# Performance work log

Hardware: AMD Instinct MI355X
Metric: run time of the kernel (lower is better)

The kernel has to match this reference:

```python
import jax, jax.numpy as jnp
import numpy as np

N = 20000   # nodes
E = 320000  # edges
F = 64      # input node features
H = 256     # hidden_layer_size
C = 10      # nbr_classes
G = 64      # graphs in the batch


def _lin(key, fan_in, fan_out):
    k1, k2 = jax.random.split(key)
    bound = 1.0 / np.sqrt(fan_in)
    W = jax.random.uniform(k1, (fan_in, fan_out), jnp.float32, -bound, bound)
    b = jax.random.uniform(k2, (fan_out,), jnp.float32, -bound, bound)
    return W, b


def setup_inputs() -> dict:
    key = jax.random.key(0)
    ks = jax.random.split(key, 10)
    x = jax.random.normal(ks[0], (N, F), jnp.float32)
    edge_index = jax.random.randint(ks[1], (2, E), 0, N)
    batch = jnp.sort(jax.random.randint(ks[2], (N,), 0, G))
    W1, b1 = _lin(ks[3], F, H)
    W2, b2 = _lin(ks[4], H, H)
    W3, b3 = _lin(ks[5], H, H)
    W4, b4 = _lin(ks[6], H, H)
    W5, b5 = _lin(ks[7], H, H)
    Wout, bout = _lin(ks[8], H, C)
    return {"x": x, "edge_index": edge_index, "batch": batch,
            "W1": W1, "b1": b1, "W2": W2, "b2": b2, "W3": W3, "b3": b3,
            "W4": W4, "b4": b4, "W5": W5, "b5": b5, "Wout": Wout, "bout": bout}


def reference(x, edge_index, batch, W1, b1, W2, b2, W3, b3, W4, b4, W5, b5, Wout, bout):
    # GCNConv (Kipf & Welling): add self-loops, D^{-1/2}(A+I)D^{-1/2} (X W) + b.
    # Dropout(p=0.5) is identity in eval mode (reference is deterministic).
    loop = jnp.arange(N)
    row = jnp.concatenate([edge_index[0], loop])  # source nodes, [E+N]
    col = jnp.concatenate([edge_index[1], loop])  # target nodes, [E+N]
    deg = jax.ops.segment_sum(jnp.ones(E + N, x.dtype), col, num_segments=N)
    dinv = jax.lax.rsqrt(deg)  # deg >= 1 thanks to self-loops
    norm = (dinv[row] * dinv[col])[:, None]  # [E+N, 1]

    def gcn_conv(h, W, b):
        m = (h @ W)[row] * norm                      # gather + normalize, [E+N, H]
        return jax.ops.segment_sum(m, col, num_segments=N) + b

    h = x
    for W, b in ((W1, b1), (W2, b2), (W3, b3), (W4, b4), (W5, b5)):
        h = jax.nn.relu(gcn_conv(h, W, b))

    # global_mean_pool over graph ids
    counts = jax.ops.segment_sum(jnp.ones(N, h.dtype), batch, num_segments=G)
    pooled = jax.ops.segment_sum(h, batch, num_segments=G) / jnp.maximum(counts, 1.0)[:, None]
    return pooled @ Wout + bout  # [G, C]
```

## Files before the change

kernel.cpp:

```cpp
#include <hip/hip_runtime.h>

#define NN 20000
#define NE 320000
#define FIN 64
#define HD 256
#define NC 10
#define NG 64
#define NB ((NN + 255) / 256)
#define EBMAX (NE + 15 * NN + 16)

typedef unsigned short u16;
typedef unsigned int u32;
typedef __attribute__((ext_vector_type(8))) short short8;
typedef __attribute__((ext_vector_type(4))) float f32x4;

__device__ __forceinline__ float bf2f(u16 u) {
    union { u32 i; float f; } v; v.i = ((u32)u) << 16; return v.f;
}
__device__ __forceinline__ u16 f2bf(float f) {
    union { float f; u32 i; } v; v.f = f;
    u32 r = v.i + 0x7fffu + ((v.i >> 16) & 1u);
    return (u16)(r >> 16);
}

__global__ void k_deg(const int* __restrict__ col, int* __restrict__ degi,
                      const int* __restrict__ batch, int* __restrict__ gstart) {
    int i = blockIdx.x * 256 + threadIdx.x;
    if (i < NE) atomicAdd(&degi[col[i]], 1);
    if (i < NN) {
        int b = batch[i];
        int prev = (i == 0) ? -1 : batch[i - 1];
        if (b != prev) gstart[b] = i;
    }
}

__global__ void k_pad(u32* __restrict__ ebuf32) {
    int i = blockIdx.x * 256 + threadIdx.x;
    if (i < EBMAX / 2) ebuf32[i] = 0x4E204E20u;
}

__global__ __launch_bounds__(256) void k_scan1(const int* __restrict__ degi,
                                               int* __restrict__ rowptr,
                                               int* __restrict__ bsum) {
    int t = threadIdx.x;
    int i = blockIdx.x * 256 + t;
    int v = (i < NN) ? ((degi[i] + 15) & ~15) : 0;
    int lane = t & 63, wid = t >> 6;
    int x = v;
#pragma unroll
    for (int off = 1; off < 64; off <<= 1) {
        int y = __shfl_up(x, off);
        if (lane >= off) x += y;
    }
    __shared__ int ws[4];
    if (lane == 63) ws[wid] = x;
    __syncthreads();
    int woff = 0;
    for (int w = 0; w < wid; ++w) woff += ws[w];
    if (i < NN) rowptr[i] = woff + x - v;
    if (t == 255) bsum[blockIdx.x] = woff + x;
}

__global__ void k_scan3(const int* __restrict__ degi, const int* __restrict__ bsum,
                        int* __restrict__ rowptr, int* __restrict__ cursor,
                        float* __restrict__ dinv,
                        const float* __restrict__ x, u16* __restrict__ u0) {
    __shared__ int pref[NB];
    if (threadIdx.x < NB) pref[threadIdx.x] = bsum[threadIdx.x];
    __syncthreads();
    if (threadIdx.x == 0) {
        int run = 0;
        for (int k = 0; k < NB; ++k) { int t = pref[k]; pref[k] = run; run += t; }
    }
    __syncthreads();
    int i = blockIdx.x * 256 + threadIdx.x;
    if (i < NN) {
        int dg = degi[i];
        int rp = rowptr[i] + pref[i >> 8];
        rowptr[i] = rp;
        cursor[i] = rp;
        dinv[i] = rsqrtf((float)(1 + dg));
        if (i == NN - 1) rowptr[NN] = rp + ((dg + 15) & ~15);
    }
    if (i < NN * FIN / 4) {
        int node = i >> 4;
        float d = rsqrtf((float)(1 + degi[node]));
        float4 v = *(const float4*)&x[(size_t)i * 4];
        u32 lo = (u32)f2bf(v.x * d) | ((u32)f2bf(v.y * d) << 16);
        u32 hi = (u32)f2bf(v.z * d) | ((u32)f2bf(v.w * d) << 16);
        *(uint2*)&u0[(size_t)i * 4] = make_uint2(lo, hi);
    }
    if (blockIdx.x == 0 && threadIdx.x < FIN) u0[(size_t)NN * FIN + threadIdx.x] = 0;
}

__global__ void k_fill(const int* __restrict__ row, const int* __restrict__ col,
                       int* __restrict__ cursor, u16* __restrict__ ebuf) {
    int e = blockIdx.x * 256 + threadIdx.x;
    if (e < NE) {
        int c = col[e];
        int pos = atomicAdd(&cursor[c], 1);
        ebuf[pos] = (u16)row[e];
    }
}

__global__ __launch_bounds__(256) void k_trans(const float* __restrict__ W0, const float* __restrict__ W1,
                                               const float* __restrict__ W2, const float* __restrict__ W3,
                                               const float* __restrict__ W4,
                                               u16* __restrict__ T0, u16* __restrict__ T1,
                                               u16* __restrict__ T2, u16* __restrict__ T3,
                                               u16* __restrict__ T4) {
    int l = blockIdx.z;
    const float* W = (l == 0) ? W0 : (l == 1) ? W1 : (l == 2) ? W2 : (l == 3) ? W3 : W4;
    u16* T = (l == 0) ? T0 : (l == 1) ? T1 : (l == 2) ? T2 : (l == 3) ? T3 : T4;
    int K = (l == 0) ? FIN : HD;
    int k0 = blockIdx.x * 32;
    if (k0 >= K) return;
    int n0 = blockIdx.y * 32;
    __shared__ float tile[32][33];
    int tx = threadIdx.x & 31, ty = threadIdx.x >> 5;
#pragma unroll
    for (int r = 0; r < 32; r += 8)
        tile[ty + r][tx] = W[(size_t)(k0 + ty + r) * HD + n0 + tx];
    __syncthreads();
#pragma unroll
    for (int r = 0; r < 32; r += 8)
        T[(size_t)(n0 + ty + r) * K + k0 + tx] = f2bf(tile[tx][ty + r]);
}

__global__ __launch_bounds__(256) void k_gatherh(const u16* __restrict__ U,
                                                 const int* __restrict__ rowptr,
                                                 const u16* __restrict__ ebuf,
                                                 const float* __restrict__ dinv,
                                                 u16* __restrict__ Z) {
    int b = blockIdx.x;
    int half = b & 1;
    int tile = b >> 1;
    int n = tile * 4 + (threadIdx.x >> 6);
    if (n >= NN) return;
    int lane = threadIdx.x & 63;
    int grp = lane >> 4;
    int seg = lane & 15;
    int fbase = half * 128 + seg * 8;
    int s = rowptr[n], e = rowptr[n + 1];
    float acc[8];
    if (grp == 0) {
        uint4 v = *(const uint4*)&U[(size_t)n * HD + fbase];
        acc[0] = bf2f((u16)(v.x & 0xffff)); acc[1] = bf2f((u16)(v.x >> 16));
        acc[2] = bf2f((u16)(v.y & 0xffff)); acc[3] = bf2f((u16)(v.y >> 16));
        acc[4] = bf2f((u16)(v.z & 0xffff)); acc[5] = bf2f((u16)(v.z >> 16));
        acc[6] = bf2f((u16)(v.w & 0xffff)); acc[7] = bf2f((u16)(v.w >> 16));
    } else {
#pragma unroll
        for (int k = 0; k < 8; ++k) acc[k] = 0.f;
    }
    for (int j = s; j < e; j += 16) {
        int myid = (lane < 16) ? (int)ebuf[j + lane] : 0;
        uint4 v[4];
#pragma unroll
        for (int k = 0; k < 4; ++k) {
            int r = __shfl(myid, grp * 4 + k);
            v[k] = *(const uint4*)&U[(size_t)r * HD + fbase];
        }
#pragma unroll
        for (int k = 0; k < 4; ++k) {
            acc[0] += bf2f((u16)(v[k].x & 0xffff)); acc[1] += bf2f((u16)(v[k].x >> 16));
            acc[2] += bf2f((u16)(v[k].y & 0xffff)); acc[3] += bf2f((u16)(v[k].y >> 16));
            acc[4] += bf2f((u16)(v[k].z & 0xffff)); acc[5] += bf2f((u16)(v[k].z >> 16));
            acc[6] += bf2f((u16)(v[k].w & 0xffff)); acc[7] += bf2f((u16)(v[k].w >> 16));
        }
    }
#pragma unroll
    for (int k = 0; k < 8; ++k) {
        acc[k] += __shfl_xor(acc[k], 16);
        acc[k] += __shfl_xor(acc[k], 32);
    }
    if (grp == 0) {
        float d = dinv[n];
        uint4 o;
        o.x = (u32)f2bf(acc[0] * d) | ((u32)f2bf(acc[1] * d) << 16);
        o.y = (u32)f2bf(acc[2] * d) | ((u32)f2bf(acc[3] * d) << 16);
        o.z = (u32)f2bf(acc[4] * d) | ((u32)f2bf(acc[5] * d) << 16);
        o.w = (u32)f2bf(acc[6] * d) | ((u32)f2bf(acc[7] * d) << 16);
        *(uint4*)&Z[(size_t)n * HD + fbase] = o;
    }
}

__global__ __launch_bounds__(256) void k_gather64(const u16* __restrict__ U,
                                                  const int* __restrict__ rowptr,
                                                  const u16* __restrict__ ebuf,
                                                  const float* __restrict__ dinv,
                                                  u16* __restrict__ Z) {
    int n = blockIdx.x * 4 + (threadIdx.x >> 6);
    if (n >= NN) return;
    int lane = threadIdx.x & 63;
    int grp = lane >> 3;
    int seg = lane & 7;
    int s = rowptr[n], e = rowptr[n + 1];
    float acc[8];
    if (grp == 0) {
        uint4 v = *(const uint4*)&U[(size_t)n * FIN + seg * 8];
        acc[0] = bf2f((u16)(v.x & 0xffff)); acc[1] = bf2f((u16)(v.x >> 16));
        acc[2] = bf2f((u16)(v.y & 0xffff)); acc[3] = bf2f((u16)(v.y >> 16));
        acc[4] = bf2f((u16)(v.z & 0xffff)); acc[5] = bf2f((u16)(v.z >> 16));
        acc[6] = bf2f((u16)(v.w & 0xffff)); acc[7] = bf2f((u16)(v.w >> 16));
    } else {
#pragma unroll
        for (int k = 0; k < 8; ++k) acc[k] = 0.f;
    }
    for (int j = s; j < e; j += 16) {
        int r0 = (int)ebuf[j + grp];
        int r1 = (int)ebuf[j + 8 + grp];
        uint4 v0 = *(const uint4*)&U[(size_t)r0 * FIN + seg * 8];
        uint4 v1 = *(const uint4*)&U[(size_t)r1 * FIN + seg * 8];
        acc[0] += bf2f((u16)(v0.x & 0xffff)); acc[1] += bf2f((u16)(v0.x >> 16));
        acc[2] += bf2f((u16)(v0.y & 0xffff)); acc[3] += bf2f((u16)(v0.y >> 16));
        acc[4] += bf2f((u16)(v0.z & 0xffff)); acc[5] += bf2f((u16)(v0.z >> 16));
        acc[6] += bf2f((u16)(v0.w & 0xffff)); acc[7] += bf2f((u16)(v0.w >> 16));
        acc[0] += bf2f((u16)(v1.x & 0xffff)); acc[1] += bf2f((u16)(v1.x >> 16));
        acc[2] += bf2f((u16)(v1.y & 0xffff)); acc[3] += bf2f((u16)(v1.y >> 16));
        acc[4] += bf2f((u16)(v1.z & 0xffff)); acc[5] += bf2f((u16)(v1.z >> 16));
        acc[6] += bf2f((u16)(v1.w & 0xffff)); acc[7] += bf2f((u16)(v1.w >> 16));
    }
#pragma unroll
    for (int off = 8; off < 64; off <<= 1)
#pragma unroll
        for (int k = 0; k < 8; ++k) acc[k] += __shfl_xor(acc[k], off);
    if (grp == 0) {
        float d = dinv[n];
        uint4 o;
        o.x = (u32)f2bf(acc[0] * d) | ((u32)f2bf(acc[1] * d) << 16);
        o.y = (u32)f2bf(acc[2] * d) | ((u32)f2bf(acc[3] * d) << 16);
        o.z = (u32)f2bf(acc[4] * d) | ((u32)f2bf(acc[5] * d) << 16);
        o.w = (u32)f2bf(acc[6] * d) | ((u32)f2bf(acc[7] * d) << 16);
        *(uint4*)&Z[(size_t)n * FIN + seg * 8] = o;
    }
}

__global__ __launch_bounds__(256) void k_mm(const u16* __restrict__ A,
                                            const u16* __restrict__ Wt,
                                            const float* __restrict__ bias,
                                            const float* __restrict__ dinv,
                                            u16* __restrict__ O,
                                            int K, int scaleOut) {
    __shared__ u16 Asm[64][40];
    __shared__ u16 Bsm[256][40];
    __shared__ float bs[HD];
    const int m0 = blockIdx.x * 64;
    const int t = threadIdx.x;
    const int wave = t >> 6;
    const int lane = t & 63;
    const int quad = lane >> 4;
    const int l16 = lane & 15;
    const int n0 = wave * 64;
    bs[t] = bias[t];
    if (blockIdx.x == 0) O[(size_t)NN * HD + t] = 0;

    f32x4 acc[4][4];
#pragma unroll
    for (int i = 0; i < 4; ++i)
#pragma unroll
        for (int j = 0; j < 4; ++j) acc[i][j] = (f32x4){0.f, 0.f, 0.f, 0.f};

    for (int k0 = 0; k0 < K; k0 += 32) {
        {
            int row = t >> 2, seg = t & 3;
            int gm = m0 + row;
            float4 v = make_float4(0.f, 0.f, 0.f, 0.f);
            if (gm < NN) v = *(const float4*)&A[(size_t)gm * K + k0 + seg * 8];
            *(float4*)&Asm[row][seg * 8] = v;
        }
        {
#pragma unroll
            for (int j = 0; j < 4; ++j) {
                float4 v = *(const float4*)&Wt[(size_t)t * K + k0 + j * 8];
                *(float4*)&Bsm[t][j * 8] = v;
            }
        }
        __syncthreads();
        short8 a[4], b[4];
#pragma unroll
        for (int i = 0; i < 4; ++i) a[i] = *(const short8*)&Asm[i * 16 + l16][quad * 8];
#pragma unroll
        for (int j = 0; j < 4; ++j) b[j] = *(const short8*)&Bsm[n0 + j * 16 + l16][quad * 8];
#pragma unroll
        for (int i = 0; i < 4; ++i)
#pragma unroll
            for (int j = 0; j < 4; ++j)
                acc[i][j] = __builtin_amdgcn_mfma_f32_16x16x32_bf16(a[i], b[j], acc[i][j], 0, 0, 0);
        __syncthreads();
    }
#pragma unroll
    for (int i = 0; i < 4; ++i) {
#pragma unroll
        for (int r = 0; r < 4; ++r) {
            int m = m0 + i * 16 + quad * 4 + r;
            if (m >= NN) continue;
            float d = scaleOut ? dinv[m] : 1.0f;
#pragma unroll
            for (int j = 0; j < 4; ++j) {
                int n = n0 + j * 16 + l16;
                float val = fmaxf(acc[i][j][r] + bs[n], 0.f) * d;
                O[(size_t)m * HD + n] = f2bf(val);
            }
        }
    }
}

__global__ __launch_bounds__(256) void k_poolout(const u16* __restrict__ h,
                                                 const int* __restrict__ gstart,
                                                 const float* __restrict__ Wout,
                                                 const float* __restrict__ bout,
                                                 float* __restrict__ out) {
    int g = blockIdx.x;
    int t = threadIdx.x;
    __shared__ float pooled[HD];
    __shared__ float part[NC][16];
    __shared__ int s_se[2];
    if (t == 0) {
        int st = gstart[g];
        int en = NN;
        for (int gg = g + 1; gg < NG; ++gg) en = min(en, gstart[gg]);
        s_se[0] = st; s_se[1] = en;
    }
    __syncthreads();
    int st = s_se[0], en = s_se[1];
    float a0 = 0.f, a1 = 0.f, a2 = 0.f, a3 = 0.f;
    int n = st;
    for (; n + 4 <= en; n += 4) {
        a0 += bf2f(h[(size_t)n * HD + t]);
        a1 += bf2f(h[(size_t)(n + 1) * HD + t]);
        a2 += bf2f(h[(size_t)(n + 2) * HD + t]);
        a3 += bf2f(h[(size_t)(n + 3) * HD + t]);
    }
    for (; n < en; ++n) a0 += bf2f(h[(size_t)n * HD + t]);
    float inv = 1.0f / (float)max(en - st, 1);
    pooled[t] = (a0 + a1 + a2 + a3) * inv;
    __syncthreads();
    if (t < NC * 16) {
        int c = t >> 4, l16 = t & 15;
        float s = 0.f;
        for (int f = l16; f < HD; f += 16)
            s = fmaf(pooled[f], Wout[(size_t)f * NC + c], s);
        part[c][l16] = s;
    }
    __syncthreads();
    if (t < NC) {
        float s = 0.f;
#pragma unroll
        for (int k = 0; k < 16; ++k) s += part[t][k];
        out[(size_t)g * NC + t] = s + bout[t];
    }
}

extern "C" void kernel_launch(void* const* d_in, const int* in_sizes, int n_in,
                              void* d_out, int out_size, void* d_ws, size_t ws_size,
                              hipStream_t stream) {
    const float* x     = (const float*)d_in[0];
    const int*   ei    = (const int*)d_in[1];
    const int*   batch = (const int*)d_in[2];
    const float* Wl[5] = {(const float*)d_in[3], (const float*)d_in[5], (const float*)d_in[7],
                          (const float*)d_in[9], (const float*)d_in[11]};
    const float* bl[5] = {(const float*)d_in[4], (const float*)d_in[6], (const float*)d_in[8],
                          (const float*)d_in[10], (const float*)d_in[12]};
    const float* Wout = (const float*)d_in[13];
    const float* bout = (const float*)d_in[14];
    float* out = (float*)d_out;

    const int* row = ei;
    const int* col = ei + NE;

    char* p = (char*)d_ws;
    auto take = [&](size_t bytes) { char* q = p; p += (bytes + 255) & ~(size_t)255; return q; };
    float* dinv   = (float*)take(NN * 4);
    int*   degi   = (int*)take(NN * 4);
    int*   rowptr = (int*)take((NN + 1) * 4);
    int*   cursor = (int*)take(NN * 4);
    int*   bsum   = (int*)take(NB * 4);
    u16*   ebuf   = (u16*)take(EBMAX * 2);
    int*   gstart = (int*)take(NG * 4);
    u16*   Wt[5];
    for (int l = 0; l < 5; ++l) Wt[l] = (u16*)take((size_t)HD * HD * 2);
    u16*   B1     = (u16*)take((size_t)(NN + 1) * HD * 2);
    u16*   B2     = (u16*)take((size_t)(NN + 1) * HD * 2);

    hipMemsetAsync(degi, 0, NN * 4, stream);
    hipMemsetAsync(gstart, 0x7F, NG * 4, stream);
    k_deg<<<(NE + 255) / 256, 256, 0, stream>>>(col, degi, batch, gstart);
    k_pad<<<(EBMAX / 2 + 255) / 256, 256, 0, stream>>>((u32*)ebuf);
    k_scan1<<<NB, 256, 0, stream>>>(degi, rowptr, bsum);
    k_scan3<<<(NN * FIN / 4 + 255) / 256, 256, 0, stream>>>(degi, bsum, rowptr, cursor, dinv, x, B1);
    k_fill<<<(NE + 255) / 256, 256, 0, stream>>>(row, col, cursor, ebuf);
    dim3 tGrid(8, 8, 5);
    k_trans<<<tGrid, 256, 0, stream>>>(Wl[0], Wl[1], Wl[2], Wl[3], Wl[4],
                                       Wt[0], Wt[1], Wt[2], Wt[3], Wt[4]);

    k_gather64<<<(NN + 3) / 4, 256, 0, stream>>>(B1, rowptr, ebuf, dinv, B2);
    k_mm<<<(NN + 63) / 64, 256, 0, stream>>>(B2, Wt[0], bl[0], dinv, B1, FIN, 1);
    const int gGrid = 2 * ((NN + 3) / 4);
    for (int l = 1; l < 5; ++l) {
        k_gatherh<<<gGrid, 256, 0, stream>>>(B1, rowptr, ebuf, dinv, B2);
        k_mm<<<(NN + 63) / 64, 256, 0, stream>>>(B2, Wt[l], bl[l], dinv, B1, HD, (l < 4) ? 1 : 0);
    }

    k_poolout<<<NG, 256, 0, stream>>>(B1, gstart, Wout, bout, out);
}
```

Baseline: 347.7 us.

## Split pooling across feature tiles and replace pad kernel with memset

The fused pool+output kernel (one block per graph) becomes a pool kernel over a graph×feature-tile grid with four node-strided row partials, followed by a separate small output kernel using one wave per (graph, class). The padding kernel for the edge buffer is replaced by a byte memset to 0x4E, so padded entries point at a dummy row index 0x4E4E = 20046 (DROW) that is zeroed and allocated. This is meant to raise parallelism in the pooling tail and drop one kernel launch, at the cost of an extra launch for the output GEMV and an intermediate pooled buffer.

```diff
diff --git a/kernel.cpp b/kernel.cpp
--- a/kernel.cpp
+++ b/kernel.cpp
@@ -8,6 +8,7 @@
 #define NG 64
 #define NB ((NN + 255) / 256)
 #define EBMAX (NE + 15 * NN + 16)
+#define DROW 20046
 
 typedef unsigned short u16;
 typedef unsigned int u32;
@@ -34,11 +35,6 @@
     }
 }
 
-__global__ void k_pad(u32* __restrict__ ebuf32) {
-    int i = blockIdx.x * 256 + threadIdx.x;
-    if (i < EBMAX / 2) ebuf32[i] = 0x4E204E20u;
-}
-
 __global__ __launch_bounds__(256) void k_scan1(const int* __restrict__ degi,
                                                int* __restrict__ rowptr,
                                                int* __restrict__ bsum) {
@@ -90,7 +86,7 @@
         u32 hi = (u32)f2bf(v.z * d) | ((u32)f2bf(v.w * d) << 16);
         *(uint2*)&u0[(size_t)i * 4] = make_uint2(lo, hi);
     }
-    if (blockIdx.x == 0 && threadIdx.x < FIN) u0[(size_t)NN * FIN + threadIdx.x] = 0;
+    if (blockIdx.x == 0 && threadIdx.x < FIN) u0[(size_t)DROW * FIN + threadIdx.x] = 0;
 }
 
 __global__ void k_fill(const int* __restrict__ row, const int* __restrict__ col,
@@ -253,7 +249,7 @@
     const int l16 = lane & 15;
     const int n0 = wave * 64;
     bs[t] = bias[t];
-    if (blockIdx.x == 0) O[(size_t)NN * HD + t] = 0;
+    if (blockIdx.x == 0) O[(size_t)DROW * HD + t] = 0;
 
     f32x4 acc[4][4];
 #pragma unroll
@@ -306,17 +302,16 @@
     }
 }
 
-__global__ __launch_bounds__(256) void k_poolout(const u16* __restrict__ h,
-                                                 const int* __restrict__ gstart,
-                                                 const float* __restrict__ Wout,
-                                                 const float* __restrict__ bout,
-                                                 float* __restrict__ out) {
+__global__ __launch_bounds__(256) void k_pool(const u16* __restrict__ h,
+                                              const int* __restrict__ gstart,
+                                              float* __restrict__ pooled) {
     int g = blockIdx.x;
-    int t = threadIdx.x;
-    __shared__ float pooled[HD];
-    __shared__ float part[NC][16];
+    int f0 = blockIdx.y * 64;
+    int tx = threadIdx.x & 63;
+    int ty = threadIdx.x >> 6;
     __shared__ int s_se[2];
-    if (t == 0) {
+    __shared__ float red[4][64];
+    if (threadIdx.x == 0) {
         int st = gstart[g];
         int en = NN;
         for (int gg = g + 1; gg < NG; ++gg) en = min(en, gstart[gg]);
@@ -324,32 +319,35 @@
     }
     __syncthreads();
     int st = s_se[0], en = s_se[1];
-    float a0 = 0.f, a1 = 0.f, a2 = 0.f, a3 = 0.f;
-    int n = st;
-    for (; n + 4 <= en; n += 4) {
-        a0 += bf2f(h[(size_t)n * HD + t]);
-        a1 += bf2f(h[(size_t)(n + 1) * HD + t]);
-        a2 += bf2f(h[(size_t)(n + 2) * HD + t]);
-        a3 += bf2f(h[(size_t)(n + 3) * HD + t]);
-    }
-    for (; n < en; ++n) a0 += bf2f(h[(size_t)n * HD + t]);
-    float inv = 1.0f / (float)max(en - st, 1);
-    pooled[t] = (a0 + a1 + a2 + a3) * inv;
-    __syncthreads();
-    if (t < NC * 16) {
-        int c = t >> 4, l16 = t & 15;
-        float s = 0.f;
-        for (int f = l16; f < HD; f += 16)
-            s = fmaf(pooled[f], Wout[(size_t)f * NC + c], s);
-        part[c][l16] = s;
-    }
-    __syncthreads();
-    if (t < NC) {
-        float s = 0.f;
-#pragma unroll
-        for (int k = 0; k < 16; ++k) s += part[t][k];
-        out[(size_t)g * NC + t] = s + bout[t];
-    }
+    float acc = 0.f;
+    for (int n = st + ty; n < en; n += 4)
+        acc += bf2f(h[(size_t)n * HD + f0 + tx]);
+    red[ty][tx] = acc;
+    __syncthreads();
+    if (ty == 0) {
+        float s = red[0][tx] + red[1][tx] + red[2][tx] + red[3][tx];
+        float inv = 1.0f / (float)max(en - st, 1);
+        pooled[(size_t)g * HD + f0 + tx] = s * inv;
+    }
+}
+
+__global__ __launch_bounds__(64) void k_out(const float* __restrict__ pooled,
+                                            const float* __restrict__ Wout,
+                                            const float* __restrict__ bout,
+                                            float* __restrict__ out) {
+    int b = blockIdx.x;
+    int g = b / NC;
+    int c = b % NC;
+    int lane = threadIdx.x;
+    float s = 0.f;
+#pragma unroll
+    for (int j = 0; j < 4; ++j) {
+        int f = lane * 4 + j;
+        s = fmaf(pooled[(size_t)g * HD + f], Wout[(size_t)f * NC + c], s);
+    }
+#pragma unroll
+    for (int off = 32; off > 0; off >>= 1) s += __shfl_down(s, off);
+    if (lane == 0) out[(size_t)g * NC + c] = s + bout[c];
 }
 
 extern "C" void kernel_launch(void* const* d_in, const int* in_sizes, int n_in,
@@ -380,13 +378,14 @@
     int*   gstart = (int*)take(NG * 4);
     u16*   Wt[5];
     for (int l = 0; l < 5; ++l) Wt[l] = (u16*)take((size_t)HD * HD * 2);
-    u16*   B1     = (u16*)take((size_t)(NN + 1) * HD * 2);
-    u16*   B2     = (u16*)take((size_t)(NN + 1) * HD * 2);
+    u16*   B1     = (u16*)take((size_t)(DROW + 1) * HD * 2);
+    u16*   B2     = (u16*)take((size_t)(DROW + 1) * HD * 2);
+    float* pooled = (float*)take(NG * HD * 4);
 
     hipMemsetAsync(degi, 0, NN * 4, stream);
     hipMemsetAsync(gstart, 0x7F, NG * 4, stream);
+    hipMemsetAsync(ebuf, 0x4E, (size_t)EBMAX * 2, stream);
     k_deg<<<(NE + 255) / 256, 256, 0, stream>>>(col, degi, batch, gstart);
-    k_pad<<<(EBMAX / 2 + 255) / 256, 256, 0, stream>>>((u32*)ebuf);
     k_scan1<<<NB, 256, 0, stream>>>(degi, rowptr, bsum);
     k_scan3<<<(NN * FIN / 4 + 255) / 256, 256, 0, stream>>>(degi, bsum, rowptr, cursor, dinv, x, B1);
     k_fill<<<(NE + 255) / 256, 256, 0, stream>>>(row, col, cursor, ebuf);
@@ -402,5 +401,7 @@
         k_mm<<<(NN + 63) / 64, 256, 0, stream>>>(B2, Wt[l], bl[l], dinv, B1, HD, (l < 4) ? 1 : 0);
     }
 
-    k_poolout<<<NG, 256, 0, stream>>>(B1, gstart, Wout, bout, out);
-}
+    dim3 poolGrid(NG, HD / 64);
+    k_pool<<<poolGrid, 256, 0, stream>>>(B1, gstart, pooled);
+    k_out<<<NG * NC, 64, 0, stream>>>(pooled, Wout, bout, out);
+}
```

Measured after the change: 349.9 us. No clear change (+0.6%).
